# Performance work log

Hardware: AMD Instinct MI355X
Metric: run time of the kernel (lower is better)

## Reference

```python
import jax, jax.numpy as jnp
import numpy as np
import math

B, S, DQ, DK, DV, H = 8, 2048, 256, 256, 256, 4
DH = DV // H
EPS = 1e-5

def _layernorm(x, g, b):
    mu = jnp.mean(x, axis=-1, keepdims=True)
    var = jnp.mean(jnp.square(x - mu), axis=-1, keepdims=True)
    return (x - mu) * jax.lax.rsqrt(var + EPS) * g + b

def setup_inputs() -> dict:
    key = jax.random.key(0)
    ks = jax.random.split(key, 12)
    s_in = 1.0 / math.sqrt(DQ)
    s_v = 1.0 / math.sqrt(DV)
    return {
        "Q": jax.random.normal(ks[0], (B, S, DQ), dtype=jnp.float32),
        "K": jax.random.normal(ks[1], (B, S, DK), dtype=jnp.float32),
        "Wq": jax.random.uniform(ks[2], (DQ, DV), jnp.float32, -s_in, s_in),
        "bq": jax.random.uniform(ks[3], (DV,), jnp.float32, -s_in, s_in),
        "Wk": jax.random.uniform(ks[4], (DK, DV), jnp.float32, -s_in, s_in),
        "bk": jax.random.uniform(ks[5], (DV,), jnp.float32, -s_in, s_in),
        "Wv": jax.random.uniform(ks[6], (DK, DV), jnp.float32, -s_in, s_in),
        "bv": jax.random.uniform(ks[7], (DV,), jnp.float32, -s_in, s_in),
        "Wo": jax.random.uniform(ks[8], (DV, DV), jnp.float32, -s_v, s_v),
        "bo": jax.random.uniform(ks[9], (DV,), jnp.float32, -s_v, s_v),
        "g0": jnp.ones((DV,), jnp.float32),
        "beta0": jnp.zeros((DV,), jnp.float32),
        "g1": jnp.ones((DV,), jnp.float32),
        "beta1": jnp.zeros((DV,), jnp.float32),
    }

def reference(Q, K, Wq, bq, Wk, bk, Wv, bv, Wo, bo, g0, beta0, g1, beta1):
    q = Q @ Wq + bq                    # [B,S,DV]
    k = K @ Wk + bk
    v = K @ Wv + bv
    q4 = q.reshape(B, S, H, DH)
    k4 = k.reshape(B, S, H, DH)
    v4 = v.reshape(B, S, H, DH)
    scores = jnp.einsum('bqhd,bkhd->bhqk', q4, k4) / math.sqrt(DH)
    A = jax.nn.softmax(scores, axis=-1)
    o = q4 + jnp.einsum('bhqk,bkhd->bqhd', A, v4)  # residual with projected Q per head
    O = o.reshape(B, S, DV)
    O = _layernorm(O, g0, beta0)
    O = O + jax.nn.relu(O @ Wo + bo)
    O = _layernorm(O, g1, beta1)
    return O
```

## Files before the change

### kernel.cpp

```cpp
#include <hip/hip_runtime.h>
#include <hip/hip_bf16.h>
#include <stdint.h>

typedef uint16_t u16;
typedef uint32_t u32;
typedef __attribute__((ext_vector_type(8))) short short8;
typedef __attribute__((ext_vector_type(4))) float f32x4;

#define LOG2E 1.44269504088896340736f

__device__ __forceinline__ u16 f2bf(float f) {
    u32 u = __builtin_bit_cast(u32, f);
    return (u16)((u + 0x7fffu + ((u >> 16) & 1u)) >> 16);
}
__device__ __forceinline__ float bf2f(u16 h) {
    u32 u = ((u32)h) << 16;
    return __builtin_bit_cast(float, u);
}
__device__ __forceinline__ u32 pack_bf16(float lo, float hi) {
    return (u32)f2bf(lo) | ((u32)f2bf(hi) << 16);
}
__device__ __forceinline__ u32 pack_bf16_fast(float lo, float hi) {
    u32 a = __builtin_bit_cast(u32, lo) + 0x8000u;
    u32 b = __builtin_bit_cast(u32, hi) + 0x8000u;
    return (a >> 16) | (b & 0xffff0000u);
}

__global__ __launch_bounds__(256)
void prep_kernel(const float* __restrict__ Q, const float* __restrict__ K,
                 u16* __restrict__ Qc, u16* __restrict__ Kc,
                 const float* __restrict__ Wq, const float* __restrict__ Wk,
                 const float* __restrict__ Wv, const float* __restrict__ Wo,
                 const float* __restrict__ bk, u16* __restrict__ WT,
                 float* __restrict__ bks) {
    const int bid = blockIdx.x;
    if (bid < 4096) {
        const float* src = (bid < 2048) ? Q : K;
        u16* dst = (bid < 2048) ? Qc : Kc;
        const size_t i = ((size_t)(bid & 2047) * 256 + threadIdx.x) * 8;
        float4 a = *(const float4*)(src + i);
        float4 b = *(const float4*)(src + i + 4);
        uint4 o;
        o.x = pack_bf16(a.x, a.y);
        o.y = pack_bf16(a.z, a.w);
        o.z = pack_bf16(b.x, b.y);
        o.w = pack_bf16(b.z, b.w);
        *(uint4*)(dst + i) = o;
    } else {
        const int idx = bid - 4096;
        const int wsel = idx >> 8, k = idx & 255, n = threadIdx.x;
        const float* W = (wsel == 0) ? Wq : (wsel == 1) ? Wk : (wsel == 2) ? Wv : Wo;
        const float scale = (wsel == 1) ? (0.125f * LOG2E) : 1.0f;
        WT[(size_t)wsel * 65536 + (size_t)n * 256 + k] = f2bf(W[(size_t)k * 256 + n] * scale);
        if (wsel == 1 && k == 0) bks[n] = bk[n] * (0.125f * LOG2E);
    }
}

__global__ __launch_bounds__(256)
void proj_kernel(const u16* __restrict__ Qc, const u16* __restrict__ Kc,
                 const u16* __restrict__ WT, const float* __restrict__ bq,
                 const float* __restrict__ bks, const float* __restrict__ bvv,
                 u16* __restrict__ qb, u16* __restrict__ kbuf, u16* __restrict__ vbuf) {
    const int z = blockIdx.z;
    const u16* A = (z == 0) ? Qc : Kc;
    const u16* BT = WT + z * 65536;
    const float* bias = (z == 0) ? bq : (z == 1) ? bks : bvv;
    u16* out = (z == 0) ? qb : (z == 1) ? kbuf : vbuf;

    __shared__ u16 As[128 * 64];
    __shared__ u16 Bs[128 * 64];
    const int tid = threadIdx.x;
    const int w = tid >> 6, lane = tid & 63;
    const int g = lane >> 4, lo = lane & 15;
    const int rowB = blockIdx.x * 128;
    const int colB = blockIdx.y * 128;
    const int wr = (w >> 1) * 64, wc = (w & 1) * 64;

    const f32x4 fz = {0.f, 0.f, 0.f, 0.f};
    f32x4 acc[4][4];
#pragma unroll
    for (int m = 0; m < 4; ++m)
#pragma unroll
        for (int n = 0; n < 4; ++n) acc[m][n] = fz;

    const int srow = tid & 127;
    const int shalf = tid >> 7;

#pragma unroll 1
    for (int kt = 0; kt < 4; ++kt) {
        const int k0 = kt * 64;
        __syncthreads();
        {
            const u16* ga = A + (size_t)(rowB + srow) * 256 + k0 + shalf * 32;
            uint4 a0 = *(const uint4*)ga;
            uint4 a1 = *(const uint4*)(ga + 8);
            uint4 a2 = *(const uint4*)(ga + 16);
            uint4 a3 = *(const uint4*)(ga + 24);
            const u16* gb = BT + (size_t)(colB + srow) * 256 + k0 + shalf * 32;
            uint4 b0 = *(const uint4*)gb;
            uint4 b1 = *(const uint4*)(gb + 8);
            uint4 b2 = *(const uint4*)(gb + 16);
            uint4 b3 = *(const uint4*)(gb + 24);
            const u32 sw = (u32)((srow & 7) << 4);
            const u32 ba = (u32)(srow * 128 + shalf * 64);
            *(uint4*)((char*)As + ((ba) ^ sw))      = a0;
            *(uint4*)((char*)As + ((ba + 16) ^ sw)) = a1;
            *(uint4*)((char*)As + ((ba + 32) ^ sw)) = a2;
            *(uint4*)((char*)As + ((ba + 48) ^ sw)) = a3;
            *(uint4*)((char*)Bs + ((ba) ^ sw))      = b0;
            *(uint4*)((char*)Bs + ((ba + 16) ^ sw)) = b1;
            *(uint4*)((char*)Bs + ((ba + 32) ^ sw)) = b2;
            *(uint4*)((char*)Bs + ((ba + 48) ^ sw)) = b3;
        }
        __syncthreads();
#pragma unroll
        for (int c = 0; c < 2; ++c) {
            short8 af[4], bfr[4];
#pragma unroll
            for (int m = 0; m < 4; ++m) {
                const int row = wr + m * 16 + lo;
                const u32 addr = (u32)(row * 128 + c * 64 + g * 16) ^ (u32)((row & 7) << 4);
                af[m] = *(const short8*)((char*)As + addr);
            }
#pragma unroll
            for (int n = 0; n < 4; ++n) {
                const int row = wc + n * 16 + lo;
                const u32 addr = (u32)(row * 128 + c * 64 + g * 16) ^ (u32)((row & 7) << 4);
                bfr[n] = *(const short8*)((char*)Bs + addr);
            }
#pragma unroll
            for (int m = 0; m < 4; ++m)
#pragma unroll
                for (int n = 0; n < 4; ++n)
                    acc[m][n] = __builtin_amdgcn_mfma_f32_16x16x32_bf16(af[m], bfr[n], acc[m][n], 0, 0, 0);
        }
    }

    float bv[4];
#pragma unroll
    for (int n = 0; n < 4; ++n) bv[n] = bias[colB + wc + n * 16 + lo];
#pragma unroll
    for (int m = 0; m < 4; ++m)
#pragma unroll
        for (int r = 0; r < 4; ++r) {
            const size_t row = (size_t)(rowB + wr + m * 16 + g * 4 + r);
#pragma unroll
            for (int n = 0; n < 4; ++n)
                out[row * 256 + colB + wc + n * 16 + lo] = f2bf(acc[m][n][r] + bv[n]);
        }
}

__global__ __launch_bounds__(512, 4)
void attn_kernel(const u16* __restrict__ qb, const u16* __restrict__ kb,
                 const u16* __restrict__ vb, u16* __restrict__ Ob) {
    __shared__ u16 Klds[2 * 64 * 64];
    __shared__ u16 Vtlds[2 * 64 * 64];
    __shared__ u16 Plds[8 * 16 * 64];
    const int tid = threadIdx.x;
    const int w = tid >> 6, lane = tid & 63;
    const int g = lane >> 4, lo = lane & 15;
    const int q0 = blockIdx.x * 128;
    const int h = blockIdx.y, b = blockIdx.z;
    const size_t hbase = (size_t)b * 2048 * 256 + (size_t)h * 64;

    short8 qf[2];
#pragma unroll
    for (int c = 0; c < 2; ++c) {
        const size_t row = (size_t)(q0 + w * 16 + lo);
        qf[c] = *(const short8*)&qb[hbase + row * 256 + c * 32 + g * 8];
    }
    const short8 vones = {0x3F80, 0x3F80, 0x3F80, 0x3F80, 0x3F80, 0x3F80, 0x3F80, 0x3F80};

    const f32x4 fz = {0.f, 0.f, 0.f, 0.f};
    f32x4 oacc[4];
#pragma unroll
    for (int n = 0; n < 4; ++n) oacc[n] = fz;
    f32x4 l_acc = fz;
    float m_run = -1e30f;

    char* Pb = (char*)Plds + w * 2048;

    const bool kRole = (tid < 256);
    const int skey = tid & 63, sseg = (tid >> 6) & 3;
    const int t4 = tid & 255;
    const int vkey = (t4 & 31) * 2, vd0 = (t4 >> 5) * 8;
    const u16* gbase;
    int goff2;
    if (kRole) { gbase = &kb[hbase + (size_t)skey * 256 + sseg * 16]; goff2 = 8; }
    else       { gbase = &vb[hbase + (size_t)vkey * 256 + vd0];       goff2 = 256; }

    uint4 s0, s1;
    auto load_tile = [&](int kt) {
        const u16* p = gbase + (size_t)kt * 16384;
        s0 = *(const uint4*)p;
        s1 = *(const uint4*)(p + goff2);
    };
    auto write_tile = [&](int sel) {
        if (kRole) {
            char* Kb_ = (char*)Klds + sel * 8192;
            const u32 sw = (u32)((skey & 7) << 4);
            const u32 ba = (u32)(skey * 128 + sseg * 32);
            *(uint4*)(Kb_ + ((ba) ^ sw)) = s0;
            *(uint4*)(Kb_ + ((ba + 16) ^ sw)) = s1;
        } else {
            char* Vb_ = (char*)Vtlds + sel * 8192;
            union { uint4 v; u16 hh[8]; } a0, a1;
            a0.v = s0; a1.v = s1;
#pragma unroll
            for (int i = 0; i < 8; ++i) {
                const int d = vd0 + i;
                const u32 addr = (u32)(d * 128 + vkey * 2) ^ (u32)((d & 7) << 4);
                *(u32*)(Vb_ + addr) = (u32)a0.hh[i] | ((u32)a1.hh[i] << 16);
            }
        }
    };

    load_tile(0);
    write_tile(0);
    load_tile(1);
    __syncthreads();

#pragma unroll 1
    for (int kt = 0; kt < 32; ++kt) {
        const int cur = kt & 1;
        char* Klb = (char*)Klds + cur * 8192;
        char* Vtb = (char*)Vtlds + cur * 8192;

        f32x4 sc[4];
#pragma unroll
        for (int km = 0; km < 4; ++km) sc[km] = fz;
        __builtin_amdgcn_s_setprio(1);
#pragma unroll
        for (int c = 0; c < 2; ++c)
#pragma unroll
            for (int km = 0; km < 4; ++km) {
                const int key = km * 16 + lo;
                const u32 addr = (u32)(key * 128 + c * 64 + g * 16) ^ (u32)((key & 7) << 4);
                const short8 kf = *(const short8*)(Klb + addr);
                sc[km] = __builtin_amdgcn_mfma_f32_16x16x32_bf16(kf, qf[c], sc[km], 0, 0, 0);
            }
        __builtin_amdgcn_s_setprio(0);

        float mt = -1e30f;
#pragma unroll
        for (int km = 0; km < 4; ++km)
#pragma unroll
            for (int r = 0; r < 4; ++r) mt = fmaxf(mt, sc[km][r]);
        mt = fmaxf(mt, __shfl_xor(mt, 16));
        mt = fmaxf(mt, __shfl_xor(mt, 32));
        if (!__all(mt <= m_run + 11.5f)) {
            const float mnew = fmaxf(m_run, mt);
            const float alpha = __builtin_amdgcn_exp2f(m_run - mnew);
#pragma unroll
            for (int r = 0; r < 4; ++r) {
                const float a = __shfl(alpha, (lane & 48) | (g * 4 + r));
                l_acc[r] *= a;
#pragma unroll
                for (int n = 0; n < 4; ++n) oacc[n][r] *= a;
            }
            m_run = mnew;
        }
#pragma unroll
        for (int km = 0; km < 4; ++km)
#pragma unroll
            for (int r = 0; r < 4; ++r)
                sc[km][r] = __builtin_amdgcn_exp2f(sc[km][r] - m_run);

        {
            const u32 sw = (u32)((lo & 7) << 4);
#pragma unroll
            for (int km = 0; km < 4; ++km) {
                uint2 val;
                val.x = pack_bf16_fast(sc[km][0], sc[km][1]);
                val.y = pack_bf16_fast(sc[km][2], sc[km][3]);
                const u32 addr = (u32)(lo * 128 + km * 32 + g * 8) ^ sw;
                *(uint2*)(Pb + addr) = val;
            }
        }

        __builtin_amdgcn_s_setprio(1);
#pragma unroll
        for (int c = 0; c < 2; ++c) {
            const u32 paddr = (u32)(lo * 128 + c * 64 + g * 16) ^ (u32)((lo & 7) << 4);
            const short8 pf = *(const short8*)(Pb + paddr);
#pragma unroll
            for (int n = 0; n < 4; ++n) {
                const int d = n * 16 + lo;
                const u32 addr = (u32)(d * 128 + c * 64 + g * 16) ^ (u32)((d & 7) << 4);
                const short8 vf = *(const short8*)(Vtb + addr);
                oacc[n] = __builtin_amdgcn_mfma_f32_16x16x32_bf16(pf, vf, oacc[n], 0, 0, 0);
            }
            l_acc = __builtin_amdgcn_mfma_f32_16x16x32_bf16(pf, vones, l_acc, 0, 0, 0);
        }
        __builtin_amdgcn_s_setprio(0);

        if (kt < 31) write_tile(cur ^ 1);
        if (kt < 30) load_tile(kt + 2);
        __syncthreads();
    }

#pragma unroll
    for (int r = 0; r < 4; ++r) {
        const float li = 1.0f / l_acc[r];
        const size_t row = (size_t)(q0 + w * 16 + g * 4 + r);
#pragma unroll
        for (int n = 0; n < 4; ++n) {
            const int d = n * 16 + lo;
            const size_t idx = hbase + row * 256 + d;
            Ob[idx] = f2bf(oacc[n][r] * li + bf2f(qb[idx]));
        }
    }
}

__global__ __launch_bounds__(256)
void ln0_kernel(const u16* in, const float* __restrict__ gam,
                const float* __restrict__ bet, float* __restrict__ of,
                u16* ob) {
    const int w = threadIdx.x >> 6, lane = threadIdx.x & 63;
    const size_t row = (size_t)blockIdx.x * 4 + w;
    const uint2 raw = *(const uint2*)(in + row * 256 + lane * 4);
    float4 v;
    v.x = bf2f((u16)(raw.x & 0xffff));
    v.y = bf2f((u16)(raw.x >> 16));
    v.z = bf2f((u16)(raw.y & 0xffff));
    v.w = bf2f((u16)(raw.y >> 16));
    float s = v.x + v.y + v.z + v.w;
    float q = v.x * v.x + v.y * v.y + v.z * v.z + v.w * v.w;
#pragma unroll
    for (int m = 1; m <= 32; m <<= 1) {
        s += __shfl_xor(s, m);
        q += __shfl_xor(q, m);
    }
    const float mu = s * (1.f / 256.f);
    const float var = q * (1.f / 256.f) - mu * mu;
    const float rstd = rsqrtf(var + 1e-5f);
    const float4 gv = ((const float4*)gam)[lane];
    const float4 bv = ((const float4*)bet)[lane];
    float4 y;
    y.x = (v.x - mu) * rstd * gv.x + bv.x;
    y.y = (v.y - mu) * rstd * gv.y + bv.y;
    y.z = (v.z - mu) * rstd * gv.z + bv.z;
    y.w = (v.w - mu) * rstd * gv.w + bv.w;
    ((float4*)(of + row * 256))[lane] = y;
    uint2 pk;
    pk.x = pack_bf16(y.x, y.y);
    pk.y = pack_bf16(y.z, y.w);
    *(uint2*)(ob + row * 256 + lane * 4) = pk;
}

__global__ __launch_bounds__(256)
void mlp_ln1_kernel(const u16* __restrict__ A, const u16* __restrict__ BT,
                    const float* __restrict__ bias, const float* __restrict__ gam,
                    const float* __restrict__ bet, float* out) {
    __shared__ char lds[40960];
    u16* As = (u16*)lds;
    u16* Bs = (u16*)(lds + 8192);
    char* Ys = lds;
    const int tid = threadIdx.x;
    const int w = tid >> 6, lane = tid & 63;
    const int g = lane >> 4, lo = lane & 15;
    const int rowB = blockIdx.x * 64;
    const int wc = w * 64;

    const f32x4 fz = {0.f, 0.f, 0.f, 0.f};
    f32x4 acc[4][4];
#pragma unroll
    for (int m = 0; m < 4; ++m)
#pragma unroll
        for (int n = 0; n < 4; ++n) acc[m][n] = fz;

    const int arow = tid & 63, aqtr = tid >> 6;
#pragma unroll 1
    for (int kt = 0; kt < 4; ++kt) {
        const int k0 = kt * 64;
        __syncthreads();
        {
            const u16* ga = A + (size_t)(rowB + arow) * 256 + k0 + aqtr * 16;
            uint4 a0 = *(const uint4*)ga;
            uint4 a1 = *(const uint4*)(ga + 8);
            const u32 swA = (u32)((arow & 7) << 4);
            const u32 baA = (u32)(arow * 128 + aqtr * 32);
            *(uint4*)((char*)As + ((baA) ^ swA))      = a0;
            *(uint4*)((char*)As + ((baA + 16) ^ swA)) = a1;
            const u16* gb = BT + (size_t)tid * 256 + k0;
            const u32 swB = (u32)((tid & 7) << 4);
            const u32 baB = (u32)(tid * 128);
#pragma unroll
            for (int j = 0; j < 8; ++j) {
                uint4 bj = *(const uint4*)(gb + j * 8);
                *(uint4*)((char*)Bs + ((baB + j * 16) ^ swB)) = bj;
            }
        }
        __syncthreads();
#pragma unroll
        for (int c = 0; c < 2; ++c) {
            short8 af[4], bfr[4];
#pragma unroll
            for (int m = 0; m < 4; ++m) {
                const int row = m * 16 + lo;
                const u32 addr = (u32)(row * 128 + c * 64 + g * 16) ^ (u32)((row & 7) << 4);
                af[m] = *(const short8*)((char*)As + addr);
            }
#pragma unroll
            for (int n = 0; n < 4; ++n) {
                const int row = wc + n * 16 + lo;
                const u32 addr = (u32)(row * 128 + c * 64 + g * 16) ^ (u32)((row & 7) << 4);
                bfr[n] = *(const short8*)((char*)Bs + addr);
            }
#pragma unroll
            for (int m = 0; m < 4; ++m)
#pragma unroll
                for (int n = 0; n < 4; ++n)
                    acc[m][n] = __builtin_amdgcn_mfma_f32_16x16x32_bf16(af[m], bfr[n], acc[m][n], 0, 0, 0);
        }
    }

    float bv[4];
#pragma unroll
    for (int n = 0; n < 4; ++n) bv[n] = bias[wc + n * 16 + lo];

    __syncthreads();

#pragma unroll
    for (int m = 0; m < 4; ++m)
#pragma unroll
        for (int r = 0; r < 4; ++r) {
            const int row_l = m * 16 + g * 4 + r;
            const u32 sw = (u32)((row_l & 7) << 4);
            const size_t grow = (size_t)(rowB + row_l);
#pragma unroll
            for (int n = 0; n < 4; ++n) {
                const int col = wc + n * 16 + lo;
                const float y = out[grow * 256 + col] + fmaxf(acc[m][n][r] + bv[n], 0.f);
                const u32 badr = (u32)(row_l * 512 + col * 2);
                const u32 addr = (badr & ~15u) ^ sw;
                *(u16*)(Ys + addr + (badr & 15u)) = f2bf(y);
            }
        }
    __syncthreads();

    {
        const int row = tid >> 2, qtr = tid & 3;
        const u32 sw = (u32)((row & 7) << 4);
        const u32 rbase = (u32)(row * 512 + qtr * 128);
        float s = 0.f, q = 0.f;
#pragma unroll
        for (int j = 0; j < 8; ++j) {
            uint4 v4 = *(const uint4*)(Ys + ((rbase + j * 16) ^ sw));
            const u32 uu[4] = {v4.x, v4.y, v4.z, v4.w};
#pragma unroll
            for (int e = 0; e < 4; ++e) {
                const float f0 = bf2f((u16)(uu[e] & 0xffff));
                const float f1 = bf2f((u16)(uu[e] >> 16));
                s += f0 + f1;
                q += f0 * f0 + f1 * f1;
            }
        }
        s += __shfl_xor(s, 1); q += __shfl_xor(q, 1);
        s += __shfl_xor(s, 2); q += __shfl_xor(q, 2);
        const float mu = s * (1.f / 256.f);
        const float var = q * (1.f / 256.f) - mu * mu;
        const float rstd = rsqrtf(var + 1e-5f);
        const size_t grow = (size_t)(rowB + row);
        float* op = out + grow * 256 + qtr * 64;
        const float* gp = gam + qtr * 64;
        const float* bp = bet + qtr * 64;
#pragma unroll
        for (int j = 0; j < 8; ++j) {
            uint4 v4 = *(const uint4*)(Ys + ((rbase + j * 16) ^ sw));
            const u32 uu[4] = {v4.x, v4.y, v4.z, v4.w};
#pragma unroll
            for (int e = 0; e < 2; ++e) {
                float4 gv = *(const float4*)(gp + j * 8 + e * 4);
                float4 bb = *(const float4*)(bp + j * 8 + e * 4);
                float4 o4;
                o4.x = (bf2f((u16)(uu[e * 2]     & 0xffff)) - mu) * rstd * gv.x + bb.x;
                o4.y = (bf2f((u16)(uu[e * 2]     >> 16))    - mu) * rstd * gv.y + bb.y;
                o4.z = (bf2f((u16)(uu[e * 2 + 1] & 0xffff)) - mu) * rstd * gv.z + bb.z;
                o4.w = (bf2f((u16)(uu[e * 2 + 1] >> 16))    - mu) * rstd * gv.w + bb.w;
                *(float4*)(op + j * 8 + e * 4) = o4;
            }
        }
    }
}

extern "C" void kernel_launch(void* const* d_in, const int* in_sizes, int n_in,
                              void* d_out, int out_size, void* d_ws, size_t ws_size,
                              hipStream_t stream) {
    const float* Q  = (const float*)d_in[0];
    const float* K  = (const float*)d_in[1];
    const float* Wq = (const float*)d_in[2];
    const float* bq = (const float*)d_in[3];
    const float* Wk = (const float*)d_in[4];
    const float* bk = (const float*)d_in[5];
    const float* Wv = (const float*)d_in[6];
    const float* bv = (const float*)d_in[7];
    const float* Wo = (const float*)d_in[8];
    const float* bo = (const float*)d_in[9];
    const float* g0 = (const float*)d_in[10];
    const float* be0 = (const float*)d_in[11];
    const float* g1 = (const float*)d_in[12];
    const float* be1 = (const float*)d_in[13];
    float* out = (float*)d_out;

    const size_t NE = (size_t)8 * 2048 * 256;
    char* ws = (char*)d_ws;
    size_t off = 0;
    auto alloc = [&](size_t bytes) { char* p = ws + off; off += (bytes + 255) & ~(size_t)255; return p; };
    u16* Qc   = (u16*)alloc(NE * 2);
    u16* Kc   = (u16*)alloc(NE * 2);
    u16* qb   = (u16*)alloc(NE * 2);
    u16* kbuf = (u16*)alloc(NE * 2);
    u16* vbuf = (u16*)alloc(NE * 2);
    u16* WT   = (u16*)alloc(4 * 65536 * 2);
    float* bks = (float*)alloc(256 * 4);
    u16* Ob16 = Qc;

    prep_kernel<<<5120, 256, 0, stream>>>(Q, K, Qc, Kc, Wq, Wk, Wv, Wo, bk, WT, bks);

    proj_kernel<<<dim3(128, 2, 3), 256, 0, stream>>>(Qc, Kc, WT, bq, bks, bv, qb, kbuf, vbuf);

    attn_kernel<<<dim3(16, 4, 8), 512, 0, stream>>>(qb, kbuf, vbuf, Ob16);

    ln0_kernel<<<4096, 256, 0, stream>>>(Ob16, g0, be0, out, Ob16);

    mlp_ln1_kernel<<<256, 256, 0, stream>>>(Ob16, WT + 3 * 65536, bo, g1, be1, out);
}
```

Measured before the change: 121.6 us.

## Fuse fp32-to-bf16 input conversion into projection GEMM and remap attention blocks per XCD

```diff
diff --git a/kernel.cpp b/kernel.cpp
--- a/kernel.cpp
+++ b/kernel.cpp
@@ -26,43 +26,24 @@
     return (a >> 16) | (b & 0xffff0000u);
 }
 
+__global__ void wt_kernel(const float* __restrict__ Wq, const float* __restrict__ Wk,
+                          const float* __restrict__ Wv, const float* __restrict__ Wo,
+                          const float* __restrict__ bk, u16* __restrict__ WT,
+                          float* __restrict__ bks) {
+    const int wsel = blockIdx.y, k = blockIdx.x, n = threadIdx.x;
+    const float* W = (wsel == 0) ? Wq : (wsel == 1) ? Wk : (wsel == 2) ? Wv : Wo;
+    const float scale = (wsel == 1) ? (0.125f * LOG2E) : 1.0f;
+    WT[(size_t)wsel * 65536 + (size_t)n * 256 + k] = f2bf(W[(size_t)k * 256 + n] * scale);
+    if (wsel == 1 && k == 0) bks[n] = bk[n] * (0.125f * LOG2E);
+}
+
 __global__ __launch_bounds__(256)
-void prep_kernel(const float* __restrict__ Q, const float* __restrict__ K,
-                 u16* __restrict__ Qc, u16* __restrict__ Kc,
-                 const float* __restrict__ Wq, const float* __restrict__ Wk,
-                 const float* __restrict__ Wv, const float* __restrict__ Wo,
-                 const float* __restrict__ bk, u16* __restrict__ WT,
-                 float* __restrict__ bks) {
-    const int bid = blockIdx.x;
-    if (bid < 4096) {
-        const float* src = (bid < 2048) ? Q : K;
-        u16* dst = (bid < 2048) ? Qc : Kc;
-        const size_t i = ((size_t)(bid & 2047) * 256 + threadIdx.x) * 8;
-        float4 a = *(const float4*)(src + i);
-        float4 b = *(const float4*)(src + i + 4);
-        uint4 o;
-        o.x = pack_bf16(a.x, a.y);
-        o.y = pack_bf16(a.z, a.w);
-        o.z = pack_bf16(b.x, b.y);
-        o.w = pack_bf16(b.z, b.w);
-        *(uint4*)(dst + i) = o;
-    } else {
-        const int idx = bid - 4096;
-        const int wsel = idx >> 8, k = idx & 255, n = threadIdx.x;
-        const float* W = (wsel == 0) ? Wq : (wsel == 1) ? Wk : (wsel == 2) ? Wv : Wo;
-        const float scale = (wsel == 1) ? (0.125f * LOG2E) : 1.0f;
-        WT[(size_t)wsel * 65536 + (size_t)n * 256 + k] = f2bf(W[(size_t)k * 256 + n] * scale);
-        if (wsel == 1 && k == 0) bks[n] = bk[n] * (0.125f * LOG2E);
-    }
-}
-
-__global__ __launch_bounds__(256)
-void proj_kernel(const u16* __restrict__ Qc, const u16* __restrict__ Kc,
+void proj_kernel(const float* __restrict__ Qf, const float* __restrict__ Kf,
                  const u16* __restrict__ WT, const float* __restrict__ bq,
                  const float* __restrict__ bks, const float* __restrict__ bvv,
                  u16* __restrict__ qb, u16* __restrict__ kbuf, u16* __restrict__ vbuf) {
     const int z = blockIdx.z;
-    const u16* A = (z == 0) ? Qc : Kc;
+    const float* Af = (z == 0) ? Qf : Kf;
     const u16* BT = WT + z * 65536;
     const float* bias = (z == 0) ? bq : (z == 1) ? bks : bvv;
     u16* out = (z == 0) ? qb : (z == 1) ? kbuf : vbuf;
@@ -91,11 +72,17 @@
         const int k0 = kt * 64;
         __syncthreads();
         {
-            const u16* ga = A + (size_t)(rowB + srow) * 256 + k0 + shalf * 32;
-            uint4 a0 = *(const uint4*)ga;
-            uint4 a1 = *(const uint4*)(ga + 8);
-            uint4 a2 = *(const uint4*)(ga + 16);
-            uint4 a3 = *(const uint4*)(ga + 24);
+            const float* ga = Af + (size_t)(rowB + srow) * 256 + k0 + shalf * 32;
+            uint4 pa[4];
+#pragma unroll
+            for (int j = 0; j < 4; ++j) {
+                float4 x = *(const float4*)(ga + j * 8);
+                float4 y = *(const float4*)(ga + j * 8 + 4);
+                pa[j].x = pack_bf16(x.x, x.y);
+                pa[j].y = pack_bf16(x.z, x.w);
+                pa[j].z = pack_bf16(y.x, y.y);
+                pa[j].w = pack_bf16(y.z, y.w);
+            }
             const u16* gb = BT + (size_t)(colB + srow) * 256 + k0 + shalf * 32;
             uint4 b0 = *(const uint4*)gb;
             uint4 b1 = *(const uint4*)(gb + 8);
@@ -103,10 +90,10 @@
             uint4 b3 = *(const uint4*)(gb + 24);
             const u32 sw = (u32)((srow & 7) << 4);
             const u32 ba = (u32)(srow * 128 + shalf * 64);
-            *(uint4*)((char*)As + ((ba) ^ sw))      = a0;
-            *(uint4*)((char*)As + ((ba + 16) ^ sw)) = a1;
-            *(uint4*)((char*)As + ((ba + 32) ^ sw)) = a2;
-            *(uint4*)((char*)As + ((ba + 48) ^ sw)) = a3;
+            *(uint4*)((char*)As + ((ba) ^ sw))      = pa[0];
+            *(uint4*)((char*)As + ((ba + 16) ^ sw)) = pa[1];
+            *(uint4*)((char*)As + ((ba + 32) ^ sw)) = pa[2];
+            *(uint4*)((char*)As + ((ba + 48) ^ sw)) = pa[3];
             *(uint4*)((char*)Bs + ((ba) ^ sw))      = b0;
             *(uint4*)((char*)Bs + ((ba + 16) ^ sw)) = b1;
             *(uint4*)((char*)Bs + ((ba + 32) ^ sw)) = b2;
@@ -159,8 +146,12 @@
     const int tid = threadIdx.x;
     const int w = tid >> 6, lane = tid & 63;
     const int g = lane >> 4, lo = lane & 15;
-    const int q0 = blockIdx.x * 128;
-    const int h = blockIdx.y, b = blockIdx.z;
+    const int bid = blockIdx.x;
+    const int xcd = bid & 7;
+    const int member = (bid >> 3) & 15;
+    const int grp = ((bid >> 7) << 3) | xcd;
+    const int q0 = member * 128;
+    const int h = grp & 3, b = grp >> 2;
     const size_t hbase = (size_t)b * 2048 * 256 + (size_t)h * 64;
 
     short8 qf[2];
@@ -507,20 +498,18 @@
     char* ws = (char*)d_ws;
     size_t off = 0;
     auto alloc = [&](size_t bytes) { char* p = ws + off; off += (bytes + 255) & ~(size_t)255; return p; };
-    u16* Qc   = (u16*)alloc(NE * 2);
-    u16* Kc   = (u16*)alloc(NE * 2);
     u16* qb   = (u16*)alloc(NE * 2);
     u16* kbuf = (u16*)alloc(NE * 2);
     u16* vbuf = (u16*)alloc(NE * 2);
     u16* WT   = (u16*)alloc(4 * 65536 * 2);
     float* bks = (float*)alloc(256 * 4);
-    u16* Ob16 = Qc;
-
-    prep_kernel<<<5120, 256, 0, stream>>>(Q, K, Qc, Kc, Wq, Wk, Wv, Wo, bk, WT, bks);
-
-    proj_kernel<<<dim3(128, 2, 3), 256, 0, stream>>>(Qc, Kc, WT, bq, bks, bv, qb, kbuf, vbuf);
-
-    attn_kernel<<<dim3(16, 4, 8), 512, 0, stream>>>(qb, kbuf, vbuf, Ob16);
+    u16* Ob16 = (u16*)alloc(NE * 2);
+
+    wt_kernel<<<dim3(256, 4), 256, 0, stream>>>(Wq, Wk, Wv, Wo, bk, WT, bks);
+
+    proj_kernel<<<dim3(128, 2, 3), 256, 0, stream>>>(Q, K, WT, bq, bks, bv, qb, kbuf, vbuf);
+
+    attn_kernel<<<512, 512, 0, stream>>>(qb, kbuf, vbuf, Ob16);
 
     ln0_kernel<<<4096, 256, 0, stream>>>(Ob16, g0, be0, out, Ob16);
 
```

New measurement: 125.7 us. 1.03x slower.
